# Optimization experiments

Hardware: AMD Instinct MI355X
Metric: run time of the kernel (lower is better)

The kernel has to match this reference:

```python
import jax, jax.numpy as jnp
import numpy as np

COMMITMENT_COST = 0.25
EPS = 1e-10


def setup_inputs() -> dict:
    key = jax.random.key(0)
    k1, k2 = jax.random.split(key)
    z_e = jax.random.normal(k1, (64, 4096, 64), dtype=jnp.float32)
    codebook = jax.random.normal(k2, (1024, 64), dtype=jnp.float32)
    return {"z_e": z_e, "codebook": codebook}


def reference(z_e, codebook):
    K, d = codebook.shape
    z_flat = z_e.reshape(-1, d)                      # [N, d]
    N = z_flat.shape[0]
    # squared L2 distances: ||z||^2 + ||e||^2 - 2 z.e  -> [N, K]
    distances = (jnp.sum(z_flat ** 2, axis=1, keepdims=True)
                 + jnp.sum(codebook ** 2, axis=1)
                 - 2.0 * jnp.matmul(z_flat, codebook.T))
    idx = jnp.argmin(distances, axis=1)              # [N]
    # direct gather (equivalent to one-hot @ codebook)
    z_q_flat = codebook[idx]                         # [N, d]
    z_q = z_q_flat.reshape(z_e.shape)
    e_latent_loss = jnp.mean((jax.lax.stop_gradient(z_q) - z_e) ** 2)
    q_latent_loss = jnp.mean((z_q - jax.lax.stop_gradient(z_e)) ** 2)
    loss = q_latent_loss + COMMITMENT_COST * e_latent_loss
    # avg one-hot probs via scatter-add (counts / N)
    counts = jnp.zeros((K,), dtype=jnp.float32).at[idx].add(1.0)
    avg_probs = counts / N
    perplexity = jnp.exp(-jnp.sum(avg_probs * jnp.log(avg_probs + EPS)))
    # straight-through estimator
    z_q_st = z_e + jax.lax.stop_gradient(z_q - z_e)
    return (z_q_st, loss, perplexity)
```

## Files before the change

### kernel.cpp

```cpp
#include <hip/hip_runtime.h>
#include <math.h>

#define NROWS   (64 * 4096)
#define D       64
#define K       1024
#define NELEM   ((size_t)NROWS * (size_t)D)

#define CHUNK_CODES 128
#define ROWB        144
#define NRM_OFF     (CHUNK_CODES * ROWB)
#define REC_USED    (NRM_OFF + 512)
#define REC_BYTES   20480
#define NCHUNK      (K / CHUNK_CODES)
#define WS_CHUNK_OFF 16384
#define WS_MAIN_NEED (WS_CHUNK_OFF + NCHUNK * REC_BYTES)
#define BLK_ROWS    256
#define NBLOCKS     (NROWS / BLK_ROWS)

#define MBIAS  256.0f
#define GAP_Q  0.4f

typedef float  f32x4  __attribute__((ext_vector_type(4)));
typedef short  s16x8  __attribute__((ext_vector_type(8)));


static __device__ inline unsigned bf16_rne(unsigned u) {
  return (u + 0x7FFFu + ((u >> 16) & 1u)) >> 16;
}
static __device__ inline unsigned umin_(unsigned a, unsigned b) { return a < b ? a : b; }
static __device__ inline unsigned umax_(unsigned a, unsigned b) { return a > b ? a : b; }

__global__ __launch_bounds__(256) void vq_prep(const float* __restrict__ cb,
                                               char* __restrict__ ws) {
  int k = blockIdx.x * 256 + threadIdx.x;
  if (k >= K) return;
  int chunk = k >> 7, cc = k & 127;
  char* rec = ws + WS_CHUNK_OFF + chunk * REC_BYTES;
  unsigned short* hrow = (unsigned short*)(rec + cc * ROWB);
  const float* src = cb + (k << 6);
  float nrm = 0.f;
  for (int j = 0; j < 64; j += 2) {
    float x0 = src[j], x1 = src[j + 1];
    nrm = fmaf(x0, x0, fmaf(x1, x1, nrm));
    unsigned h0 = bf16_rne(__float_as_uint(x0));
    unsigned h1 = bf16_rne(__float_as_uint(x1));
    *(unsigned*)(hrow + j) = h0 | (h1 << 16);
  }
  *(float*)(rec + NRM_OFF + cc * 4) = nrm + MBIAS;
}

__global__ __launch_bounds__(256, 4) void vq_mfma(const float* __restrict__ z,
                                                  const float* __restrict__ cb,
                                                  const char* __restrict__ ws,
                                                  float* __restrict__ zq,
                                                  unsigned int* __restrict__ counts,
                                                  float* __restrict__ block_loss) {
  __shared__ __align__(16) char sblob[REC_BYTES];

  const int t    = threadIdx.x;
  const int w    = t >> 6;
  const int lane = t & 63;
  const int g    = lane >> 4;
  const int ln16 = lane & 15;

  const int rowbase = blockIdx.x * BLK_ROWS + w * 64;
  s16x8 zh[4][2];
#pragma unroll
  for (int rt = 0; rt < 4; ++rt) {
    int row = rowbase + rt * 16 + ln16;
    const float4* zr = (const float4*)(z + (size_t)row * 64);
#pragma unroll
    for (int ks = 0; ks < 2; ++ks) {
      float4 a = zr[ks * 8 + g * 2];
      float4 b = zr[ks * 8 + g * 2 + 1];
      s16x8 hh;
      hh[0] = (short)bf16_rne(__float_as_uint(a.x));
      hh[1] = (short)bf16_rne(__float_as_uint(a.y));
      hh[2] = (short)bf16_rne(__float_as_uint(a.z));
      hh[3] = (short)bf16_rne(__float_as_uint(a.w));
      hh[4] = (short)bf16_rne(__float_as_uint(b.x));
      hh[5] = (short)bf16_rne(__float_as_uint(b.y));
      hh[6] = (short)bf16_rne(__float_as_uint(b.z));
      hh[7] = (short)bf16_rne(__float_as_uint(b.w));
      zh[rt][ks] = hh;
    }
  }

  unsigned q1[4] = {~0u, ~0u, ~0u, ~0u};
  unsigned q2[4] = {~0u, ~0u, ~0u, ~0u};
  unsigned q3[4] = {~0u, ~0u, ~0u, ~0u};

  const int aoff = ln16 * ROWB + g * 16;

#define LD_TILE(TL, E0, E1, NR) {                                             \
    const char* _ab = sblob + (TL) * (16 * ROWB) + aoff;                      \
    E0 = *(const s16x8*)(_ab);                                                \
    E1 = *(const s16x8*)(_ab + 64);                                           \
    NR = *(const f32x4*)(sblob + NRM_OFF + (TL) * 64 + (g << 4)); }

  for (int c = 0; c < NCHUNK; ++c) {
    __syncthreads();
    {
      const float4* src = (const float4*)(ws + WS_CHUNK_OFF + c * REC_BYTES);
      float4* dst = (float4*)sblob;
#pragma unroll
      for (int i = 0; i < 5; ++i) {
        int idx = t + 256 * i;
        dst[idx] = src[idx];
      }
    }
    __syncthreads();

    s16x8 e0a, e1a; f32x4 nra;
    LD_TILE(0, e0a, e1a, nra)
#pragma unroll
    for (int tl = 0; tl < 8; ++tl) {
      s16x8 e0b, e1b; f32x4 nrb;
      if (tl < 7) { LD_TILE(tl + 1, e0b, e1b, nrb) }

      f32x4 ac0 = {0.f,0.f,0.f,0.f}, ac1 = {0.f,0.f,0.f,0.f};
      f32x4 ac2 = {0.f,0.f,0.f,0.f}, ac3 = {0.f,0.f,0.f,0.f};
      ac0 = __builtin_amdgcn_mfma_f32_16x16x32_bf16(e0a, zh[0][0], ac0, 0, 0, 0);
      ac1 = __builtin_amdgcn_mfma_f32_16x16x32_bf16(e0a, zh[1][0], ac1, 0, 0, 0);
      ac2 = __builtin_amdgcn_mfma_f32_16x16x32_bf16(e0a, zh[2][0], ac2, 0, 0, 0);
      ac3 = __builtin_amdgcn_mfma_f32_16x16x32_bf16(e0a, zh[3][0], ac3, 0, 0, 0);
      ac0 = __builtin_amdgcn_mfma_f32_16x16x32_bf16(e1a, zh[0][1], ac0, 0, 0, 0);
      ac1 = __builtin_amdgcn_mfma_f32_16x16x32_bf16(e1a, zh[1][1], ac1, 0, 0, 0);
      ac2 = __builtin_amdgcn_mfma_f32_16x16x32_bf16(e1a, zh[2][1], ac2, 0, 0, 0);
      ac3 = __builtin_amdgcn_mfma_f32_16x16x32_bf16(e1a, zh[3][1], ac3, 0, 0, 0);

      const unsigned kb = (unsigned)((c << 7) + (tl << 4) + (g << 2));
#define UPDP(RT, R) {                                                         \
        float m = fmaf(-2.f, ac##RT[R], nra[R]);                              \
        unsigned key = (__float_as_uint(m) & 0xFFFFFC00u) | (kb + R);         \
        unsigned t1 = umax_(q1[RT], key); q1[RT] = umin_(q1[RT], key);        \
        unsigned t2 = umax_(q2[RT], t1);  q2[RT] = umin_(q2[RT], t1);         \
        q3[RT] = umin_(q3[RT], t2); }
      UPDP(0, 0) UPDP(1, 0) UPDP(2, 0) UPDP(3, 0)
      UPDP(0, 1) UPDP(1, 1) UPDP(2, 1) UPDP(3, 1)
      UPDP(0, 2) UPDP(1, 2) UPDP(2, 2) UPDP(3, 2)
      UPDP(0, 3) UPDP(1, 3) UPDP(2, 3) UPDP(3, 3)
#undef UPDP
      if (tl < 7) { e0a = e0b; e1a = e1b; nra = nrb; }
    }
  }

  __syncthreads();
  int*   sk  = (int*)sblob;
  float* red = (float*)(sblob + 1024);

  const float4* cb4 = (const float4*)cb;
  const float4* z4g = (const float4*)z;

#pragma unroll
  for (int rt = 0; rt < 4; ++rt) {
    unsigned a1 = q1[rt], a2 = q2[rt], a3 = q3[rt];
#pragma unroll
    for (int dx = 16; dx <= 32; dx <<= 1) {
      unsigned b1 = (unsigned)__shfl_xor((int)a1, dx);
      unsigned b2 = (unsigned)__shfl_xor((int)a2, dx);
      unsigned b3 = (unsigned)__shfl_xor((int)a3, dx);
      unsigned x  = umax_(a1, b1);
      a1 = umin_(a1, b1);
      unsigned y  = umin_(a2, b2);
      unsigned zz = umax_(a2, b2);
      unsigned w3 = umin_(a3, b3);
      a2 = umin_(x, y);
      a3 = umin_(umax_(x, y), umin_(zz, w3));
    }
    int   i1 = (int)(a1 & 1023u), i2 = (int)(a2 & 1023u);
    float f1 = __uint_as_float(a1 & 0xFFFFFC00u);
    float f2 = __uint_as_float(a2 & 0xFFFFFC00u);
    float f3 = __uint_as_float(a3 & 0xFFFFFC00u);
    bool needFull = (f3 - f1) < GAP_Q;
    bool needPair = !needFull && ((f2 - f1) < GAP_Q);
    int  kstar = i1;

    if (g == 0) {
      int row = rowbase + rt * 16 + ln16;
      if (needPair) {
        float d1 = 0.f, d2 = 0.f;
        const float4* zr = z4g + (size_t)row * 16;
        const float4* c1 = cb4 + i1 * 16;
        const float4* c2 = cb4 + i2 * 16;
#pragma unroll
        for (int j = 0; j < 16; ++j) {
          float4 zv = zr[j], a = c1[j], b = c2[j];
          float e;
          e = zv.x - a.x; d1 = fmaf(e, e, d1);
          e = zv.y - a.y; d1 = fmaf(e, e, d1);
          e = zv.z - a.z; d1 = fmaf(e, e, d1);
          e = zv.w - a.w; d1 = fmaf(e, e, d1);
          e = zv.x - b.x; d2 = fmaf(e, e, d2);
          e = zv.y - b.y; d2 = fmaf(e, e, d2);
          e = zv.z - b.z; d2 = fmaf(e, e, d2);
          e = zv.w - b.w; d2 = fmaf(e, e, d2);
        }
        if (d2 < d1 || (d2 == d1 && i2 < i1)) kstar = i2;
      }
      if (!needFull) {
        sk[w * 64 + rt * 16 + ln16] = kstar;
        atomicAdd(&counts[kstar], 1u);
      }
    }

    unsigned long long fullmask = __ballot(needFull && g == 0);
    while (fullmask) {
      int src = __ffsll(fullmask) - 1;
      fullmask &= fullmask - 1;
      int lrow = w * 64 + rt * 16 + src;
      int row  = blockIdx.x * BLK_ROWS + lrow;
      const float4* zr = z4g + (size_t)row * 16;
      float bv = 3.4e38f; int bi = 0;
      for (int c16 = 0; c16 < 16; ++c16) {
        int code = c16 * 64 + lane;
        const float4* cr = cb4 + code * 16;
        float d = 0.f;
#pragma unroll
        for (int j = 0; j < 16; ++j) {
          float4 zv = zr[j], cv = cr[j];
          float e;
          e = zv.x - cv.x; d = fmaf(e, e, d);
          e = zv.y - cv.y; d = fmaf(e, e, d);
          e = zv.z - cv.z; d = fmaf(e, e, d);
          e = zv.w - cv.w; d = fmaf(e, e, d);
        }
        if (d < bv) { bv = d; bi = code; }
      }
#pragma unroll
      for (int dx = 1; dx < 64; dx <<= 1) {
        float ov = __shfl_xor(bv, dx); int oi = __shfl_xor(bi, dx);
        if (ov < bv || (ov == bv && oi < bi)) { bv = ov; bi = oi; }
      }
      if (lane == 0) { sk[lrow] = bi; atomicAdd(&counts[bi], 1u); }
    }
  }

  __syncthreads();

  float lpart = 0.f;
  const int base4 = blockIdx.x * (BLK_ROWS * 16);
  float4* out4 = (float4*)zq;
#pragma unroll
  for (int i = 0; i < 16; ++i) {
    int idx = t + 256 * i;
    int row = idx >> 4, c4 = idx & 15;
    int kk = sk[row];
    float4 cv = cb4[kk * 16 + c4];
    float4 zv = z4g[base4 + idx];
    float e;
    e = zv.x - cv.x; lpart = fmaf(e, e, lpart);
    e = zv.y - cv.y; lpart = fmaf(e, e, lpart);
    e = zv.z - cv.z; lpart = fmaf(e, e, lpart);
    e = zv.w - cv.w; lpart = fmaf(e, e, lpart);
    out4[base4 + idx] = cv;
  }
  red[t] = lpart;
  __syncthreads();
#pragma unroll
  for (int s = 128; s > 0; s >>= 1) {
    if (t < s) red[t] += red[t + s];
    __syncthreads();
  }
  if (t == 0) block_loss[blockIdx.x] = red[0];
}

__global__ __launch_bounds__(1024) void vq_finalize(const unsigned int* __restrict__ counts,
                                                    const float* __restrict__ block_loss,
                                                    float* __restrict__ out, int nb) {
  __shared__ float sh[1024];
  __shared__ float sl[1024];
  const int t = threadIdx.x;
  float c = (float)counts[t];
  float p = c * (1.0f / (float)NROWS);
  sh[t] = p * logf(p + 1e-10f);
  float bl = (t < nb) ? block_loss[t] : 0.f;
  sl[t] = bl;
  __syncthreads();
#pragma unroll
  for (int s = 512; s > 0; s >>= 1) {
    if (t < s) { sh[t] += sh[t + s]; sl[t] += sl[t + s]; }
    __syncthreads();
  }
  if (t == 0) {
    out[NELEM]     = 1.25f * sl[0] / (float)NELEM;
    out[NELEM + 1] = expf(-sh[0]);
  }
}

#define DOT4(acc, a, e) \
  acc = fmaf((a).x, (e).x, fmaf((a).y, (e).y, fmaf((a).z, (e).z, fmaf((a).w, (e).w, (acc)))))
#define SQD4(acc, a, e) { \
  float _dx = (e).x - (a).x, _dy = (e).y - (a).y, _dz = (e).z - (a).z, _dw = (e).w - (a).w; \
  acc = fmaf(_dx, _dx, fmaf(_dy, _dy, fmaf(_dz, _dz, fmaf(_dw, _dw, (acc))))); }

__global__ __launch_bounds__(256) void vq_norms_fb(const float* __restrict__ cb,
                                                   float* __restrict__ norms) {
  int k = blockIdx.x * blockDim.x + threadIdx.x;
  if (k >= K) return;
  const float4* e4 = (const float4*)(cb + (k << 6));
  float a0 = 0.f, a1 = 0.f, a2 = 0.f, a3 = 0.f;
#pragma unroll
  for (int j = 0; j < 16; j += 4) {
    float4 e;
    e = e4[j + 0]; DOT4(a0, e, e);
    e = e4[j + 1]; DOT4(a1, e, e);
    e = e4[j + 2]; DOT4(a2, e, e);
    e = e4[j + 3]; DOT4(a3, e, e);
  }
  norms[k] = (a0 + a1) + (a2 + a3);
}

__global__ __launch_bounds__(256) void vq_main_fb(const float* __restrict__ z,
                                                  const float* __restrict__ cb,
                                                  const float* __restrict__ norms,
                                                  float* __restrict__ zq,
                                                  unsigned int* __restrict__ counts,
                                                  float* __restrict__ block_loss) {
  const int tid = threadIdx.x;
  const int row = blockIdx.x * 256 + tid;
  const float4* zr4 = (const float4*)(z + (size_t)row * D);
  float4 zr[16];
#pragma unroll
  for (int j = 0; j < 16; ++j) zr[j] = zr4[j];
  float best = 3.4e38f;
  int   bidx = 0;
  for (int k = 0; k < K; k += 2) {
    const float4* e0 = (const float4*)(cb + (k << 6));
    const float4* e1 = e0 + 16;
    float a0 = 0.f, a1 = 0.f, a2 = 0.f, a3 = 0.f;
    float b0 = 0.f, b1 = 0.f, b2 = 0.f, b3 = 0.f;
#pragma unroll
    for (int j = 0; j < 16; j += 4) {
      float4 tt;
      tt = e0[j + 0]; DOT4(a0, zr[j + 0], tt);
      tt = e1[j + 0]; DOT4(b0, zr[j + 0], tt);
      tt = e0[j + 1]; DOT4(a1, zr[j + 1], tt);
      tt = e1[j + 1]; DOT4(b1, zr[j + 1], tt);
      tt = e0[j + 2]; DOT4(a2, zr[j + 2], tt);
      tt = e1[j + 2]; DOT4(b2, zr[j + 2], tt);
      tt = e0[j + 3]; DOT4(a3, zr[j + 3], tt);
      tt = e1[j + 3]; DOT4(b3, zr[j + 3], tt);
    }
    float d0 = (a0 + a1) + (a2 + a3);
    float d1 = (b0 + b1) + (b2 + b3);
    float m0 = fmaf(-2.f, d0, norms[k]);
    float m1 = fmaf(-2.f, d1, norms[k + 1]);
    if (m0 < best) { best = m0; bidx = k; }
    if (m1 < best) { best = m1; bidx = k + 1; }
  }
  const float4* eb4 = (const float4*)(cb + ((size_t)bidx << 6));
  float4* o4 = (float4*)(zq + (size_t)row * D);
  float l0 = 0.f, l1 = 0.f, l2 = 0.f, l3 = 0.f;
#pragma unroll
  for (int j = 0; j < 16; j += 4) {
    float4 e;
    e = eb4[j + 0]; o4[j + 0] = e; SQD4(l0, zr[j + 0], e);
    e = eb4[j + 1]; o4[j + 1] = e; SQD4(l1, zr[j + 1], e);
    e = eb4[j + 2]; o4[j + 2] = e; SQD4(l2, zr[j + 2], e);
    e = eb4[j + 3]; o4[j + 3] = e; SQD4(l3, zr[j + 3], e);
  }
  float row_loss = (l0 + l1) + (l2 + l3);
  atomicAdd(&counts[bidx], 1u);
  __shared__ float redf[256];
  redf[tid] = row_loss;
  __syncthreads();
#pragma unroll
  for (int s = 128; s > 0; s >>= 1) {
    if (tid < s) redf[tid] += redf[tid + s];
    __syncthreads();
  }
  if (tid == 0) block_loss[blockIdx.x] = redf[0];
}

extern "C" void kernel_launch(void* const* d_in, const int* in_sizes, int n_in,
                              void* d_out, int out_size, void* d_ws, size_t ws_size,
                              hipStream_t stream) {
  const float* z  = (const float*)d_in[0];
  const float* cb = (const float*)d_in[1];
  float* out = (float*)d_out;

  unsigned int* counts     = (unsigned int*)d_ws;
  float*        block_loss = (float*)((char*)d_ws + 4096);

  hipMemsetAsync(d_ws, 0, 4096, stream);

  if (ws_size >= WS_MAIN_NEED) {
    vq_prep<<<dim3(4), dim3(256), 0, stream>>>(cb, (char*)d_ws);
    vq_mfma<<<dim3(NBLOCKS), dim3(256), 0, stream>>>(z, cb, (const char*)d_ws,
                                                     out, counts, block_loss);
    vq_finalize<<<dim3(1), dim3(1024), 0, stream>>>(counts, block_loss, out, NBLOCKS);
  } else {
    float* norms = (float*)((char*)d_ws + 12288);
    vq_norms_fb<<<dim3(4), dim3(256), 0, stream>>>(cb, norms);
    vq_main_fb<<<dim3(NROWS / 256), dim3(256), 0, stream>>>(z, cb, norms,
                                                            out, counts, block_loss);
    vq_finalize<<<dim3(1), dim3(1024), 0, stream>>>(counts, block_loss, out, 1024);
  }
}
```

Before: 246.0 us.

## Double-buffer codebook chunks in LDS and fold norm bias into MFMA accumulator

Codebook chunks now go into two LDS buffers. The next chunk's global loads are issued into registers before the current chunk's MFMA loop and written to the other buffer afterwards, so one barrier per chunk replaces two and load latency overlaps with compute. The prep kernel pre-scales the bf16 codebook by -2, and the MFMA accumulators start from the norm vector, which removes the per-element fma in the argmin update. GAP_Q is raised from 0.4 to 0.8 to allow for the different rounding: scaling by -2 before bf16 changes precision slightly, so the gap widens the set of candidates sent for exact re-check. LDS use doubles to about 40KB per block, which may limit occupancy at the declared 4 blocks per CU.

```diff
diff --git a/kernel.cpp b/kernel.cpp
--- a/kernel.cpp
+++ b/kernel.cpp
@@ -9,7 +9,6 @@
 #define CHUNK_CODES 128
 #define ROWB        144
 #define NRM_OFF     (CHUNK_CODES * ROWB)
-#define REC_USED    (NRM_OFF + 512)
 #define REC_BYTES   20480
 #define NCHUNK      (K / CHUNK_CODES)
 #define WS_CHUNK_OFF 16384
@@ -18,7 +17,7 @@
 #define NBLOCKS     (NROWS / BLK_ROWS)
 
 #define MBIAS  256.0f
-#define GAP_Q  0.4f
+#define GAP_Q  0.8f
 
 typedef float  f32x4  __attribute__((ext_vector_type(4)));
 typedef short  s16x8  __attribute__((ext_vector_type(8)));
@@ -42,8 +41,8 @@
   for (int j = 0; j < 64; j += 2) {
     float x0 = src[j], x1 = src[j + 1];
     nrm = fmaf(x0, x0, fmaf(x1, x1, nrm));
-    unsigned h0 = bf16_rne(__float_as_uint(x0));
-    unsigned h1 = bf16_rne(__float_as_uint(x1));
+    unsigned h0 = bf16_rne(__float_as_uint(-2.f * x0));
+    unsigned h1 = bf16_rne(__float_as_uint(-2.f * x1));
     *(unsigned*)(hrow + j) = h0 | (h1 << 16);
   }
   *(float*)(rec + NRM_OFF + cc * 4) = nrm + MBIAS;
@@ -55,7 +54,7 @@
                                                   float* __restrict__ zq,
                                                   unsigned int* __restrict__ counts,
                                                   float* __restrict__ block_loss) {
-  __shared__ __align__(16) char sblob[REC_BYTES];
+  __shared__ __align__(16) char sblob[2][REC_BYTES];
 
   const int t    = threadIdx.x;
   const int w    = t >> 6;
@@ -92,34 +91,39 @@
 
   const int aoff = ln16 * ROWB + g * 16;
 
-#define LD_TILE(TL, E0, E1, NR) {                                             \
-    const char* _ab = sblob + (TL) * (16 * ROWB) + aoff;                      \
+#define LD_TILE(BUF, TL, E0, E1, NR) {                                        \
+    const char* _ab = (BUF) + (TL) * (16 * ROWB) + aoff;                      \
     E0 = *(const s16x8*)(_ab);                                                \
     E1 = *(const s16x8*)(_ab + 64);                                           \
-    NR = *(const f32x4*)(sblob + NRM_OFF + (TL) * 64 + (g << 4)); }
+    NR = *(const f32x4*)((BUF) + NRM_OFF + (TL) * 64 + (g << 4)); }
+
+  const float4* wsrc = (const float4*)(ws + WS_CHUNK_OFF);
+  {
+    float4 s0 = wsrc[t], s1 = wsrc[t + 256], s2 = wsrc[t + 512],
+           s3 = wsrc[t + 768], s4 = wsrc[t + 1024];
+    float4* dst = (float4*)sblob[0];
+    dst[t] = s0; dst[t + 256] = s1; dst[t + 512] = s2;
+    dst[t + 768] = s3; dst[t + 1024] = s4;
+  }
+  __syncthreads();
 
   for (int c = 0; c < NCHUNK; ++c) {
-    __syncthreads();
-    {
-      const float4* src = (const float4*)(ws + WS_CHUNK_OFF + c * REC_BYTES);
-      float4* dst = (float4*)sblob;
-#pragma unroll
-      for (int i = 0; i < 5; ++i) {
-        int idx = t + 256 * i;
-        dst[idx] = src[idx];
-      }
-    }
-    __syncthreads();
+    const char* buf = sblob[c & 1];
+    float4 s0, s1, s2, s3, s4;
+    if (c < NCHUNK - 1) {
+      const float4* src = wsrc + (size_t)(c + 1) * (REC_BYTES / 16);
+      s0 = src[t]; s1 = src[t + 256]; s2 = src[t + 512];
+      s3 = src[t + 768]; s4 = src[t + 1024];
+    }
 
     s16x8 e0a, e1a; f32x4 nra;
-    LD_TILE(0, e0a, e1a, nra)
+    LD_TILE(buf, 0, e0a, e1a, nra)
 #pragma unroll
     for (int tl = 0; tl < 8; ++tl) {
       s16x8 e0b, e1b; f32x4 nrb;
-      if (tl < 7) { LD_TILE(tl + 1, e0b, e1b, nrb) }
-
-      f32x4 ac0 = {0.f,0.f,0.f,0.f}, ac1 = {0.f,0.f,0.f,0.f};
-      f32x4 ac2 = {0.f,0.f,0.f,0.f}, ac3 = {0.f,0.f,0.f,0.f};
+      if (tl < 7) { LD_TILE(buf, tl + 1, e0b, e1b, nrb) }
+
+      f32x4 ac0 = nra, ac1 = nra, ac2 = nra, ac3 = nra;
       ac0 = __builtin_amdgcn_mfma_f32_16x16x32_bf16(e0a, zh[0][0], ac0, 0, 0, 0);
       ac1 = __builtin_amdgcn_mfma_f32_16x16x32_bf16(e0a, zh[1][0], ac1, 0, 0, 0);
       ac2 = __builtin_amdgcn_mfma_f32_16x16x32_bf16(e0a, zh[2][0], ac2, 0, 0, 0);
@@ -131,8 +135,7 @@
 
       const unsigned kb = (unsigned)((c << 7) + (tl << 4) + (g << 2));
 #define UPDP(RT, R) {                                                         \
-        float m = fmaf(-2.f, ac##RT[R], nra[R]);                              \
-        unsigned key = (__float_as_uint(m) & 0xFFFFFC00u) | (kb + R);         \
+        unsigned key = (__float_as_uint(ac##RT[R]) & 0xFFFFFC00u) | (kb + R); \
         unsigned t1 = umax_(q1[RT], key); q1[RT] = umin_(q1[RT], key);        \
         unsigned t2 = umax_(q2[RT], t1);  q2[RT] = umin_(q2[RT], t1);         \
         q3[RT] = umin_(q3[RT], t2); }
@@ -143,11 +146,17 @@
 #undef UPDP
       if (tl < 7) { e0a = e0b; e1a = e1b; nra = nrb; }
     }
-  }
-
-  __syncthreads();
-  int*   sk  = (int*)sblob;
-  float* red = (float*)(sblob + 1024);
+
+    if (c < NCHUNK - 1) {
+      float4* dst = (float4*)sblob[(c + 1) & 1];
+      dst[t] = s0; dst[t + 256] = s1; dst[t + 512] = s2;
+      dst[t + 768] = s3; dst[t + 1024] = s4;
+    }
+    __syncthreads();
+  }
+
+  int*   sk  = (int*)sblob[0];
+  float* red = (float*)(sblob[0] + 1024);
 
   const float4* cb4 = (const float4*)cb;
   const float4* z4g = (const float4*)z;
```

After: 513.8 us. +108.9%, slower.

## Fold -2 scale into codebook and norm into MFMA accumulator; halve block rows

Applied to the files above, without the earlier changes.

The prep kernel now stores the bf16 codebook pre-scaled by -2, and each MFMA accumulator starts from the code norms, so the per-candidate fma is removed from the top-3 selection loop. Block size drops from 256 to 128 rows, so each wave handles 32 rows and there are twice as many blocks, and finalize sums the extra block-loss entries. The ambiguity gap threshold is doubled to allow for the changed rounding, which may send more rows to the exact fallback path. Halving rows per block also halves reuse of each codebook chunk staged in shared memory.

```diff
diff --git a/kernel.cpp b/kernel.cpp
--- a/kernel.cpp
+++ b/kernel.cpp
@@ -9,16 +9,15 @@
 #define CHUNK_CODES 128
 #define ROWB        144
 #define NRM_OFF     (CHUNK_CODES * ROWB)
-#define REC_USED    (NRM_OFF + 512)
 #define REC_BYTES   20480
 #define NCHUNK      (K / CHUNK_CODES)
 #define WS_CHUNK_OFF 16384
 #define WS_MAIN_NEED (WS_CHUNK_OFF + NCHUNK * REC_BYTES)
-#define BLK_ROWS    256
+#define BLK_ROWS    128
 #define NBLOCKS     (NROWS / BLK_ROWS)
 
 #define MBIAS  256.0f
-#define GAP_Q  0.4f
+#define GAP_Q  0.8f
 
 typedef float  f32x4  __attribute__((ext_vector_type(4)));
 typedef short  s16x8  __attribute__((ext_vector_type(8)));
@@ -42,8 +41,8 @@
   for (int j = 0; j < 64; j += 2) {
     float x0 = src[j], x1 = src[j + 1];
     nrm = fmaf(x0, x0, fmaf(x1, x1, nrm));
-    unsigned h0 = bf16_rne(__float_as_uint(x0));
-    unsigned h1 = bf16_rne(__float_as_uint(x1));
+    unsigned h0 = bf16_rne(__float_as_uint(-2.f * x0));
+    unsigned h1 = bf16_rne(__float_as_uint(-2.f * x1));
     *(unsigned*)(hrow + j) = h0 | (h1 << 16);
   }
   *(float*)(rec + NRM_OFF + cc * 4) = nrm + MBIAS;
@@ -63,10 +62,10 @@
   const int g    = lane >> 4;
   const int ln16 = lane & 15;
 
-  const int rowbase = blockIdx.x * BLK_ROWS + w * 64;
-  s16x8 zh[4][2];
-#pragma unroll
-  for (int rt = 0; rt < 4; ++rt) {
+  const int rowbase = blockIdx.x * BLK_ROWS + w * 32;
+  s16x8 zh[2][2];
+#pragma unroll
+  for (int rt = 0; rt < 2; ++rt) {
     int row = rowbase + rt * 16 + ln16;
     const float4* zr = (const float4*)(z + (size_t)row * 64);
 #pragma unroll
@@ -86,9 +85,9 @@
     }
   }
 
-  unsigned q1[4] = {~0u, ~0u, ~0u, ~0u};
-  unsigned q2[4] = {~0u, ~0u, ~0u, ~0u};
-  unsigned q3[4] = {~0u, ~0u, ~0u, ~0u};
+  unsigned q1[2] = {~0u, ~0u};
+  unsigned q2[2] = {~0u, ~0u};
+  unsigned q3[2] = {~0u, ~0u};
 
   const int aoff = ln16 * ROWB + g * 16;
 
@@ -98,10 +97,12 @@
     E1 = *(const s16x8*)(_ab + 64);                                           \
     NR = *(const f32x4*)(sblob + NRM_OFF + (TL) * 64 + (g << 4)); }
 
+  const float4* wsrc = (const float4*)(ws + WS_CHUNK_OFF);
+
   for (int c = 0; c < NCHUNK; ++c) {
     __syncthreads();
     {
-      const float4* src = (const float4*)(ws + WS_CHUNK_OFF + c * REC_BYTES);
+      const float4* src = wsrc + (size_t)c * (REC_BYTES / 16);
       float4* dst = (float4*)sblob;
 #pragma unroll
       for (int i = 0; i < 5; ++i) {
@@ -118,28 +119,22 @@
       s16x8 e0b, e1b; f32x4 nrb;
       if (tl < 7) { LD_TILE(tl + 1, e0b, e1b, nrb) }
 
-      f32x4 ac0 = {0.f,0.f,0.f,0.f}, ac1 = {0.f,0.f,0.f,0.f};
-      f32x4 ac2 = {0.f,0.f,0.f,0.f}, ac3 = {0.f,0.f,0.f,0.f};
+      f32x4 ac0 = nra, ac1 = nra;
       ac0 = __builtin_amdgcn_mfma_f32_16x16x32_bf16(e0a, zh[0][0], ac0, 0, 0, 0);
       ac1 = __builtin_amdgcn_mfma_f32_16x16x32_bf16(e0a, zh[1][0], ac1, 0, 0, 0);
-      ac2 = __builtin_amdgcn_mfma_f32_16x16x32_bf16(e0a, zh[2][0], ac2, 0, 0, 0);
-      ac3 = __builtin_amdgcn_mfma_f32_16x16x32_bf16(e0a, zh[3][0], ac3, 0, 0, 0);
       ac0 = __builtin_amdgcn_mfma_f32_16x16x32_bf16(e1a, zh[0][1], ac0, 0, 0, 0);
       ac1 = __builtin_amdgcn_mfma_f32_16x16x32_bf16(e1a, zh[1][1], ac1, 0, 0, 0);
-      ac2 = __builtin_amdgcn_mfma_f32_16x16x32_bf16(e1a, zh[2][1], ac2, 0, 0, 0);
-      ac3 = __builtin_amdgcn_mfma_f32_16x16x32_bf16(e1a, zh[3][1], ac3, 0, 0, 0);
 
       const unsigned kb = (unsigned)((c << 7) + (tl << 4) + (g << 2));
 #define UPDP(RT, R) {                                                         \
-        float m = fmaf(-2.f, ac##RT[R], nra[R]);                              \
-        unsigned key = (__float_as_uint(m) & 0xFFFFFC00u) | (kb + R);         \
+        unsigned key = (__float_as_uint(ac##RT[R]) & 0xFFFFFC00u) | (kb + R); \
         unsigned t1 = umax_(q1[RT], key); q1[RT] = umin_(q1[RT], key);        \
         unsigned t2 = umax_(q2[RT], t1);  q2[RT] = umin_(q2[RT], t1);         \
         q3[RT] = umin_(q3[RT], t2); }
-      UPDP(0, 0) UPDP(1, 0) UPDP(2, 0) UPDP(3, 0)
-      UPDP(0, 1) UPDP(1, 1) UPDP(2, 1) UPDP(3, 1)
-      UPDP(0, 2) UPDP(1, 2) UPDP(2, 2) UPDP(3, 2)
-      UPDP(0, 3) UPDP(1, 3) UPDP(2, 3) UPDP(3, 3)
+      UPDP(0, 0) UPDP(1, 0)
+      UPDP(0, 1) UPDP(1, 1)
+      UPDP(0, 2) UPDP(1, 2)
+      UPDP(0, 3) UPDP(1, 3)
 #undef UPDP
       if (tl < 7) { e0a = e0b; e1a = e1b; nra = nrb; }
     }
@@ -147,13 +142,13 @@
 
   __syncthreads();
   int*   sk  = (int*)sblob;
-  float* red = (float*)(sblob + 1024);
+  float* red = (float*)(sblob + 512);
 
   const float4* cb4 = (const float4*)cb;
   const float4* z4g = (const float4*)z;
 
 #pragma unroll
-  for (int rt = 0; rt < 4; ++rt) {
+  for (int rt = 0; rt < 2; ++rt) {
     unsigned a1 = q1[rt], a2 = q2[rt], a3 = q3[rt];
 #pragma unroll
     for (int dx = 16; dx <= 32; dx <<= 1) {
@@ -199,7 +194,7 @@
         if (d2 < d1 || (d2 == d1 && i2 < i1)) kstar = i2;
       }
       if (!needFull) {
-        sk[w * 64 + rt * 16 + ln16] = kstar;
+        sk[w * 32 + rt * 16 + ln16] = kstar;
         atomicAdd(&counts[kstar], 1u);
       }
     }
@@ -208,7 +203,7 @@
     while (fullmask) {
       int src = __ffsll(fullmask) - 1;
       fullmask &= fullmask - 1;
-      int lrow = w * 64 + rt * 16 + src;
+      int lrow = w * 32 + rt * 16 + src;
       int row  = blockIdx.x * BLK_ROWS + lrow;
       const float4* zr = z4g + (size_t)row * 16;
       float bv = 3.4e38f; int bi = 0;
@@ -242,7 +237,7 @@
   const int base4 = blockIdx.x * (BLK_ROWS * 16);
   float4* out4 = (float4*)zq;
 #pragma unroll
-  for (int i = 0; i < 16; ++i) {
+  for (int i = 0; i < 8; ++i) {
     int idx = t + 256 * i;
     int row = idx >> 4, c4 = idx & 15;
     int kk = sk[row];
@@ -275,6 +270,7 @@
   float p = c * (1.0f / (float)NROWS);
   sh[t] = p * logf(p + 1e-10f);
   float bl = (t < nb) ? block_loss[t] : 0.f;
+  if (t + 1024 < nb) bl += block_loss[t + 1024];
   sl[t] = bl;
   __syncthreads();
 #pragma unroll
```

Result: slower. 364.5 us (+48.2%).

## Fold norm and -2 scale into MFMA, split top-3 tracking into two chains

Applied to the files above, without the earlier changes.

The codebook is pre-scaled by -2 before bf16 conversion, and the MFMA accumulators are seeded with the code norms, so the distance comes out of the MFMA without a separate fma. Top-3 tracking is split into two independent register sets, merged at the end, to shorten the dependency chains. The refinement gap threshold is doubled to absorb the extra rounding, which sends more rows to exact recheck, and launch bounds drop to 2 blocks per CU to allow more registers.

```diff
diff --git a/kernel.cpp b/kernel.cpp
--- a/kernel.cpp
+++ b/kernel.cpp
@@ -9,7 +9,6 @@
 #define CHUNK_CODES 128
 #define ROWB        144
 #define NRM_OFF     (CHUNK_CODES * ROWB)
-#define REC_USED    (NRM_OFF + 512)
 #define REC_BYTES   20480
 #define NCHUNK      (K / CHUNK_CODES)
 #define WS_CHUNK_OFF 16384
@@ -18,7 +17,7 @@
 #define NBLOCKS     (NROWS / BLK_ROWS)
 
 #define MBIAS  256.0f
-#define GAP_Q  0.4f
+#define GAP_Q  0.8f
 
 typedef float  f32x4  __attribute__((ext_vector_type(4)));
 typedef short  s16x8  __attribute__((ext_vector_type(8)));
@@ -42,14 +41,14 @@
   for (int j = 0; j < 64; j += 2) {
     float x0 = src[j], x1 = src[j + 1];
     nrm = fmaf(x0, x0, fmaf(x1, x1, nrm));
-    unsigned h0 = bf16_rne(__float_as_uint(x0));
-    unsigned h1 = bf16_rne(__float_as_uint(x1));
+    unsigned h0 = bf16_rne(__float_as_uint(-2.f * x0));
+    unsigned h1 = bf16_rne(__float_as_uint(-2.f * x1));
     *(unsigned*)(hrow + j) = h0 | (h1 << 16);
   }
   *(float*)(rec + NRM_OFF + cc * 4) = nrm + MBIAS;
 }
 
-__global__ __launch_bounds__(256, 4) void vq_mfma(const float* __restrict__ z,
+__global__ __launch_bounds__(256, 2) void vq_mfma(const float* __restrict__ z,
                                                   const float* __restrict__ cb,
                                                   const char* __restrict__ ws,
                                                   float* __restrict__ zq,
@@ -86,9 +85,8 @@
     }
   }
 
-  unsigned q1[4] = {~0u, ~0u, ~0u, ~0u};
-  unsigned q2[4] = {~0u, ~0u, ~0u, ~0u};
-  unsigned q3[4] = {~0u, ~0u, ~0u, ~0u};
+  unsigned qa1[4] = {~0u, ~0u, ~0u, ~0u}, qa2[4] = {~0u, ~0u, ~0u, ~0u}, qa3[4] = {~0u, ~0u, ~0u, ~0u};
+  unsigned qb1[4] = {~0u, ~0u, ~0u, ~0u}, qb2[4] = {~0u, ~0u, ~0u, ~0u}, qb3[4] = {~0u, ~0u, ~0u, ~0u};
 
   const int aoff = ln16 * ROWB + g * 16;
 
@@ -98,10 +96,12 @@
     E1 = *(const s16x8*)(_ab + 64);                                           \
     NR = *(const f32x4*)(sblob + NRM_OFF + (TL) * 64 + (g << 4)); }
 
+  const float4* wsrc = (const float4*)(ws + WS_CHUNK_OFF);
+
   for (int c = 0; c < NCHUNK; ++c) {
     __syncthreads();
     {
-      const float4* src = (const float4*)(ws + WS_CHUNK_OFF + c * REC_BYTES);
+      const float4* src = wsrc + (size_t)c * (REC_BYTES / 16);
       float4* dst = (float4*)sblob;
 #pragma unroll
       for (int i = 0; i < 5; ++i) {
@@ -118,8 +118,7 @@
       s16x8 e0b, e1b; f32x4 nrb;
       if (tl < 7) { LD_TILE(tl + 1, e0b, e1b, nrb) }
 
-      f32x4 ac0 = {0.f,0.f,0.f,0.f}, ac1 = {0.f,0.f,0.f,0.f};
-      f32x4 ac2 = {0.f,0.f,0.f,0.f}, ac3 = {0.f,0.f,0.f,0.f};
+      f32x4 ac0 = nra, ac1 = nra, ac2 = nra, ac3 = nra;
       ac0 = __builtin_amdgcn_mfma_f32_16x16x32_bf16(e0a, zh[0][0], ac0, 0, 0, 0);
       ac1 = __builtin_amdgcn_mfma_f32_16x16x32_bf16(e0a, zh[1][0], ac1, 0, 0, 0);
       ac2 = __builtin_amdgcn_mfma_f32_16x16x32_bf16(e0a, zh[2][0], ac2, 0, 0, 0);
@@ -130,16 +129,15 @@
       ac3 = __builtin_amdgcn_mfma_f32_16x16x32_bf16(e1a, zh[3][1], ac3, 0, 0, 0);
 
       const unsigned kb = (unsigned)((c << 7) + (tl << 4) + (g << 2));
-#define UPDP(RT, R) {                                                         \
-        float m = fmaf(-2.f, ac##RT[R], nra[R]);                              \
-        unsigned key = (__float_as_uint(m) & 0xFFFFFC00u) | (kb + R);         \
-        unsigned t1 = umax_(q1[RT], key); q1[RT] = umin_(q1[RT], key);        \
-        unsigned t2 = umax_(q2[RT], t1);  q2[RT] = umin_(q2[RT], t1);         \
-        q3[RT] = umin_(q3[RT], t2); }
-      UPDP(0, 0) UPDP(1, 0) UPDP(2, 0) UPDP(3, 0)
-      UPDP(0, 1) UPDP(1, 1) UPDP(2, 1) UPDP(3, 1)
-      UPDP(0, 2) UPDP(1, 2) UPDP(2, 2) UPDP(3, 2)
-      UPDP(0, 3) UPDP(1, 3) UPDP(2, 3) UPDP(3, 3)
+#define UPDP(Q1, Q2, Q3, RT, R) {                                             \
+        unsigned key = (__float_as_uint(ac##RT[R]) & 0xFFFFFC00u) | (kb + R); \
+        unsigned t1 = umax_(Q1[RT], key); Q1[RT] = umin_(Q1[RT], key);        \
+        unsigned t2 = umax_(Q2[RT], t1);  Q2[RT] = umin_(Q2[RT], t1);         \
+        Q3[RT] = umin_(Q3[RT], t2); }
+      UPDP(qa1, qa2, qa3, 0, 0) UPDP(qa1, qa2, qa3, 1, 0) UPDP(qa1, qa2, qa3, 2, 0) UPDP(qa1, qa2, qa3, 3, 0)
+      UPDP(qb1, qb2, qb3, 0, 2) UPDP(qb1, qb2, qb3, 1, 2) UPDP(qb1, qb2, qb3, 2, 2) UPDP(qb1, qb2, qb3, 3, 2)
+      UPDP(qa1, qa2, qa3, 0, 1) UPDP(qa1, qa2, qa3, 1, 1) UPDP(qa1, qa2, qa3, 2, 1) UPDP(qa1, qa2, qa3, 3, 1)
+      UPDP(qb1, qb2, qb3, 0, 3) UPDP(qb1, qb2, qb3, 1, 3) UPDP(qb1, qb2, qb3, 2, 3) UPDP(qb1, qb2, qb3, 3, 3)
 #undef UPDP
       if (tl < 7) { e0a = e0b; e1a = e1b; nra = nrb; }
     }
@@ -154,7 +152,17 @@
 
 #pragma unroll
   for (int rt = 0; rt < 4; ++rt) {
-    unsigned a1 = q1[rt], a2 = q2[rt], a3 = q3[rt];
+    unsigned a1 = qa1[rt], a2 = qa2[rt], a3 = qa3[rt];
+    {
+      unsigned b1 = qb1[rt], b2 = qb2[rt], b3 = qb3[rt];
+      unsigned x  = umax_(a1, b1);
+      a1 = umin_(a1, b1);
+      unsigned y  = umin_(a2, b2);
+      unsigned zz = umax_(a2, b2);
+      unsigned w3 = umin_(a3, b3);
+      a2 = umin_(x, y);
+      a3 = umin_(umax_(x, y), umin_(zz, w3));
+    }
 #pragma unroll
     for (int dx = 16; dx <= 32; dx <<= 1) {
       unsigned b1 = (unsigned)__shfl_xor((int)a1, dx);
```

Result: slower. 398.5 us (+62.0%).
